# Kernel optimization log

Hardware: AMD Instinct MI355X
Metric: run time of the kernel (lower is better)

The kernel has to match this reference:

```python
import jax, jax.numpy as jnp
import numpy as np

EPS_T = 0.008856  # CIE threshold


def _f(t):
    # torch.where(t > 0.008856, t**(1/3), 7.787*t + 16/116)
    safe = jnp.where(t > EPS_T, t, 1.0)  # avoid nan/inf grads in untaken branch
    return jnp.where(t > EPS_T, jnp.cbrt(safe), 7.787 * t + 16.0 / 116.0)


def rgb_to_cieluv(rgb):
    # rgb: (N, 3, H, W) -> (N, 3, H, W) with channels (L, u, v)
    r, g, b = rgb[:, 0], rgb[:, 1], rgb[:, 2]
    x = 0.4124564 * r + 0.3575761 * g + 0.1804375 * b
    y = 0.2126729 * r + 0.7151522 * g + 0.072175 * b
    z = 0.0193339 * r + 0.119192 * g + 0.9503041 * b
    x = x / 0.95047
    z = z / 1.08883
    fx, fy, fz = _f(x), _f(y), _f(z)
    l = 116.0 * fy - 16.0
    u = 13.0 * l * (fx - fy)
    v = 13.0 * l * (fy - fz)
    return jnp.stack([l, u, v], axis=1)


def box_filter(img, patch_size):
    # depthwise all-ones conv, same padding as torch (pad = k//2)
    c = img.shape[1]
    kernel = jnp.ones((c, 1, patch_size, patch_size), img.dtype)
    pad = patch_size // 2
    return jax.lax.conv_general_dilated(
        img, kernel, window_strides=(1, 1),
        padding=[(pad, pad), (pad, pad)], feature_group_count=c)


def setup_inputs() -> dict:
    key = jax.random.key(0)
    k1, k2 = jax.random.split(key)
    N, C, H, W = 16, 3, 512, 512
    inp = jax.random.uniform(k1, (N, C, H, W), dtype=jnp.float32)
    tgt = jax.random.uniform(k2, (N, C, H, W), dtype=jnp.float32)
    return {"input": inp, "target": tgt, "patch_size": 15}


def reference(input, target, patch_size):
    a = box_filter(rgb_to_cieluv(input), patch_size)
    b = box_filter(rgb_to_cieluv(target), patch_size)
    # l_loss + u_loss + v_loss: per-channel MSE, summed across channels
    per_channel_mse = jnp.mean((a - b) ** 2, axis=(0, 2, 3))
    return per_channel_mse.sum()
```

## Files before the change

kernel.cpp:

```cpp
#include <hip/hip_runtime.h>
#include <math.h>

#define IMG_W 512
#define IMG_H 512
#define NIMG 16
#define HWSZ (IMG_W * IMG_H)
#define CHWSZ (3 * HWSZ)
#define NORM (1.0 / 4194304.0)
#define NBLK_V 1536

__device__ __forceinline__ float f_lab(float t) {
    float c = exp2f(log2f(t) * (1.0f / 3.0f));
    return (t > 0.008856f) ? c : fmaf(7.787f, t, 0.13793103448275862f);
}

__device__ __forceinline__ void rgb_to_luv(float r, float g, float b,
                                           float& l, float& u, float& v) {
    float x = 0.4124564f * r + 0.3575761f * g + 0.1804375f * b;
    float y = 0.2126729f * r + 0.7151522f * g + 0.0721750f * b;
    float z = 0.0193339f * r + 0.1191920f * g + 0.9503041f * b;
    x *= (1.0f / 0.95047f);
    z *= (1.0f / 1.08883f);
    float fx = f_lab(x), fy = f_lab(y), fz = f_lab(z);
    l = 116.0f * fy - 16.0f;
    u = 13.0f * l * (fx - fy);
    v = 13.0f * l * (fy - fz);
}

__device__ __forceinline__ unsigned short f2bf(float x) {
    unsigned int u = __float_as_uint(x);
    u += 0x7fff + ((u >> 16) & 1);
    return (unsigned short)(u >> 16);
}

__device__ __forceinline__ void hslide(const float d[8], float o[8], int lane) {
    float L[7], R[7];
    #pragma unroll
    for (int j = 0; j < 7; ++j) {
        float l = __shfl_up(d[j + 1], 1, 64);
        L[j] = (lane == 0) ? 0.0f : l;
        float r = __shfl_down(d[j], 1, 64);
        R[j] = (lane == 63) ? 0.0f : r;
    }
    float s = 0.0f;
    #pragma unroll
    for (int j = 0; j < 7; ++j) s += L[j];
    #pragma unroll
    for (int j = 0; j < 8; ++j) s += d[j];
    o[0] = s;
    #pragma unroll
    for (int k = 1; k < 8; ++k) o[k] = o[k - 1] + R[k - 1] - L[k - 1];
}

__device__ __forceinline__ uint4 pack8(const float o[8]) {
    uint4 p;
    p.x = (unsigned)f2bf(o[0]) | ((unsigned)f2bf(o[1]) << 16);
    p.y = (unsigned)f2bf(o[2]) | ((unsigned)f2bf(o[3]) << 16);
    p.z = (unsigned)f2bf(o[4]) | ((unsigned)f2bf(o[5]) << 16);
    p.w = (unsigned)f2bf(o[6]) | ((unsigned)f2bf(o[7]) << 16);
    return p;
}

__global__ __launch_bounds__(256) void luv_hpass3(
        const float* __restrict__ inp, const float* __restrict__ tgt,
        unsigned short* __restrict__ tmp) {
    int blk = blockIdx.x;
    int n = blk >> 7;
    int lane = threadIdx.x & 63;
    int h = ((blk & 127) << 2) | (threadIdx.x >> 6);
    int w0 = lane << 3;
    size_t base = (size_t)n * CHWSZ + (size_t)h * IMG_W + w0;

    float dl[8], du[8], dv[8];
    {
        float R[8], G[8], B[8];
        *(float4*)&R[0] = *(const float4*)(inp + base);
        *(float4*)&R[4] = *(const float4*)(inp + base + 4);
        *(float4*)&G[0] = *(const float4*)(inp + base + HWSZ);
        *(float4*)&G[4] = *(const float4*)(inp + base + HWSZ + 4);
        *(float4*)&B[0] = *(const float4*)(inp + base + 2 * HWSZ);
        *(float4*)&B[4] = *(const float4*)(inp + base + 2 * HWSZ + 4);
        #pragma unroll
        for (int j = 0; j < 8; ++j)
            rgb_to_luv(R[j], G[j], B[j], dl[j], du[j], dv[j]);
        *(float4*)&R[0] = *(const float4*)(tgt + base);
        *(float4*)&R[4] = *(const float4*)(tgt + base + 4);
        *(float4*)&G[0] = *(const float4*)(tgt + base + HWSZ);
        *(float4*)&G[4] = *(const float4*)(tgt + base + HWSZ + 4);
        *(float4*)&B[0] = *(const float4*)(tgt + base + 2 * HWSZ);
        *(float4*)&B[4] = *(const float4*)(tgt + base + 2 * HWSZ + 4);
        #pragma unroll
        for (int j = 0; j < 8; ++j) {
            float l2, u2, v2;
            rgb_to_luv(R[j], G[j], B[j], l2, u2, v2);
            dl[j] -= l2; du[j] -= u2; dv[j] -= v2;
        }
    }

    float o[8];
    hslide(dl, o, lane);
    *reinterpret_cast<uint4*>(tmp + base) = pack8(o);
    hslide(du, o, lane);
    *reinterpret_cast<uint4*>(tmp + base + HWSZ) = pack8(o);
    hslide(dv, o, lane);
    *reinterpret_cast<uint4*>(tmp + base + 2 * HWSZ) = pack8(o);
}

__device__ __forceinline__ void unpack8(uint4 v, float f[8]) {
    f[0] = __uint_as_float(v.x << 16);
    f[1] = __uint_as_float(v.x & 0xffff0000u);
    f[2] = __uint_as_float(v.y << 16);
    f[3] = __uint_as_float(v.y & 0xffff0000u);
    f[4] = __uint_as_float(v.z << 16);
    f[5] = __uint_as_float(v.z & 0xffff0000u);
    f[6] = __uint_as_float(v.w << 16);
    f[7] = __uint_as_float(v.w & 0xffff0000u);
}

template <bool GLO>
__device__ __forceinline__ void vprime(const unsigned short* __restrict__ col,
                                       int h0, float W[8]) {
    #pragma unroll
    for (int j = 0; j < 15; ++j) {
        int h = h0 - 7 + j;
        if (GLO && h < 0) continue;
        uint4 v = *(const uint4*)(col + (size_t)h * IMG_W);
        float a[8];
        unpack8(v, a);
        #pragma unroll
        for (int c = 0; c < 8; ++c) W[c] += a[c];
    }
}

template <bool GLO, bool GHI>
__device__ __forceinline__ void vchunk8(const unsigned short* __restrict__ col,
                                        int hb, float W[8], float& acc) {
    const uint4 z = make_uint4(0u, 0u, 0u, 0u);
    uint4 va[8], vs[8];
    #pragma unroll
    for (int j = 0; j < 8; ++j) {
        int ha = hb + j + 8, hs = hb + j - 7;
        va[j] = (GHI && ha >= IMG_H) ? z : *(const uint4*)(col + (size_t)ha * IMG_W);
        vs[j] = (GLO && hs < 0)      ? z : *(const uint4*)(col + (size_t)hs * IMG_W);
    }
    #pragma unroll
    for (int j = 0; j < 8; ++j) {
        float a[8], s[8];
        unpack8(va[j], a);
        unpack8(vs[j], s);
        #pragma unroll
        for (int c = 0; c < 8; ++c) {
            acc += W[c] * W[c];
            W[c] += a[c] - s[c];
        }
    }
}

__global__ __launch_bounds__(64) void vpass3(
        const unsigned short* __restrict__ tmp, float* __restrict__ partial) {
    int blk = blockIdx.x;
    int hseg = blk & 31;
    int nc = blk >> 5;
    int t = threadIdx.x;
    const unsigned short* col = tmp + (size_t)nc * HWSZ + (t << 3);
    int h0 = hseg << 4;

    float W[8] = {0.f, 0.f, 0.f, 0.f, 0.f, 0.f, 0.f, 0.f};
    float acc = 0.0f;

    if (hseg == 0) {
        vprime<true>(col, h0, W);
        vchunk8<true, false>(col, h0, W, acc);
        vchunk8<false, false>(col, h0 + 8, W, acc);
    } else if (hseg == 31) {
        vprime<false>(col, h0, W);
        vchunk8<false, false>(col, h0, W, acc);
        vchunk8<false, true>(col, h0 + 8, W, acc);
    } else {
        vprime<false>(col, h0, W);
        vchunk8<false, false>(col, h0, W, acc);
        vchunk8<false, false>(col, h0 + 8, W, acc);
    }

    #pragma unroll
    for (int off = 32; off > 0; off >>= 1)
        acc += __shfl_down(acc, off, 64);
    if (t == 0) partial[blk] = acc;
}

__global__ __launch_bounds__(256) void finalize3(
        const float* __restrict__ partial, float* __restrict__ out) {
    int t = threadIdx.x;
    float a = 0.0f;
    #pragma unroll
    for (int i = 0; i < NBLK_V; i += 256) a += partial[i + t];
    #pragma unroll
    for (int off = 32; off > 0; off >>= 1)
        a += __shfl_down(a, off, 64);
    __shared__ float red[4];
    int lane = t & 63, wid = t >> 6;
    if (lane == 0) red[wid] = a;
    __syncthreads();
    if (t == 0)
        out[0] = (float)((double)(red[0] + red[1] + red[2] + red[3]) * NORM);
}

extern "C" void kernel_launch(void* const* d_in, const int* in_sizes, int n_in,
                              void* d_out, int out_size, void* d_ws, size_t ws_size,
                              hipStream_t stream) {
    const float* inp = (const float*)d_in[0];
    const float* tgt = (const float*)d_in[1];
    float* out = (float*)d_out;
    float* partial = (float*)d_ws;
    unsigned short* tmp = (unsigned short*)((char*)d_ws + 8192);

    luv_hpass3<<<NIMG * 128, 256, 0, stream>>>(inp, tgt, tmp);
    vpass3<<<NBLK_V, 64, 0, stream>>>(tmp, partial);
    finalize3<<<1, 256, 0, stream>>>(partial, out);
}
```

Before: 133.6 us.

## Fuse LUV conversion and box filter into one kernel with shared-memory ring

Merges the horizontal-pass and vertical-pass kernels into one kernel. Each block converts rows to LUV differences, horizontally box-filters them into a bf16 ring buffer in LDS, and slides the vertical window there. This removes the global bf16 intermediate write and its repeated reads, plus one launch. In exchange it recomputes halo rows per 32-row tile, launches only 256 large blocks, and adds block-wide barriers inside the loop.

```diff
diff --git a/kernel.cpp b/kernel.cpp
--- a/kernel.cpp
+++ b/kernel.cpp
@@ -7,7 +7,8 @@
 #define HWSZ (IMG_W * IMG_H)
 #define CHWSZ (3 * HWSZ)
 #define NORM (1.0 / 4194304.0)
-#define NBLK_V 1536
+#define RING 24
+#define NBLK 256
 
 __device__ __forceinline__ float f_lab(float t) {
     float c = exp2f(log2f(t) * (1.0f / 3.0f));
@@ -32,6 +33,9 @@
     u += 0x7fff + ((u >> 16) & 1);
     return (unsigned short)(u >> 16);
 }
+__device__ __forceinline__ float bf2f(unsigned short u) {
+    return __uint_as_float((unsigned)u << 16);
+}
 
 __device__ __forceinline__ void hslide(const float d[8], float o[8], int lane) {
     float L[7], R[7];
@@ -61,139 +65,126 @@
     return p;
 }
 
-__global__ __launch_bounds__(256) void luv_hpass3(
-        const float* __restrict__ inp, const float* __restrict__ tgt,
-        unsigned short* __restrict__ tmp) {
-    int blk = blockIdx.x;
-    int n = blk >> 7;
-    int lane = threadIdx.x & 63;
-    int h = ((blk & 127) << 2) | (threadIdx.x >> 6);
+__device__ __forceinline__ void load6(const float* __restrict__ p, size_t base,
+                                      float4 v[6]) {
+    v[0] = *(const float4*)(p + base);
+    v[1] = *(const float4*)(p + base + 4);
+    v[2] = *(const float4*)(p + base + HWSZ);
+    v[3] = *(const float4*)(p + base + HWSZ + 4);
+    v[4] = *(const float4*)(p + base + 2 * HWSZ);
+    v[5] = *(const float4*)(p + base + 2 * HWSZ + 4);
+}
+
+__device__ __forceinline__ void row_to_ring(const float4 vi[6], const float4 vt[6],
+        bool valid, unsigned short (*ring)[3][IMG_W], int slot, int lane) {
     int w0 = lane << 3;
-    size_t base = (size_t)n * CHWSZ + (size_t)h * IMG_W + w0;
-
-    float dl[8], du[8], dv[8];
-    {
-        float R[8], G[8], B[8];
-        *(float4*)&R[0] = *(const float4*)(inp + base);
-        *(float4*)&R[4] = *(const float4*)(inp + base + 4);
-        *(float4*)&G[0] = *(const float4*)(inp + base + HWSZ);
-        *(float4*)&G[4] = *(const float4*)(inp + base + HWSZ + 4);
-        *(float4*)&B[0] = *(const float4*)(inp + base + 2 * HWSZ);
-        *(float4*)&B[4] = *(const float4*)(inp + base + 2 * HWSZ + 4);
+    if (valid) {
+        float R[8], G[8], B[8], dl[8], du[8], dv[8];
+        *(float4*)&R[0] = vi[0]; *(float4*)&R[4] = vi[1];
+        *(float4*)&G[0] = vi[2]; *(float4*)&G[4] = vi[3];
+        *(float4*)&B[0] = vi[4]; *(float4*)&B[4] = vi[5];
         #pragma unroll
         for (int j = 0; j < 8; ++j)
             rgb_to_luv(R[j], G[j], B[j], dl[j], du[j], dv[j]);
-        *(float4*)&R[0] = *(const float4*)(tgt + base);
-        *(float4*)&R[4] = *(const float4*)(tgt + base + 4);
-        *(float4*)&G[0] = *(const float4*)(tgt + base + HWSZ);
-        *(float4*)&G[4] = *(const float4*)(tgt + base + HWSZ + 4);
-        *(float4*)&B[0] = *(const float4*)(tgt + base + 2 * HWSZ);
-        *(float4*)&B[4] = *(const float4*)(tgt + base + 2 * HWSZ + 4);
+        *(float4*)&R[0] = vt[0]; *(float4*)&R[4] = vt[1];
+        *(float4*)&G[0] = vt[2]; *(float4*)&G[4] = vt[3];
+        *(float4*)&B[0] = vt[4]; *(float4*)&B[4] = vt[5];
         #pragma unroll
         for (int j = 0; j < 8; ++j) {
             float l2, u2, v2;
             rgb_to_luv(R[j], G[j], B[j], l2, u2, v2);
             dl[j] -= l2; du[j] -= u2; dv[j] -= v2;
         }
-    }
-
-    float o[8];
-    hslide(dl, o, lane);
-    *reinterpret_cast<uint4*>(tmp + base) = pack8(o);
-    hslide(du, o, lane);
-    *reinterpret_cast<uint4*>(tmp + base + HWSZ) = pack8(o);
-    hslide(dv, o, lane);
-    *reinterpret_cast<uint4*>(tmp + base + 2 * HWSZ) = pack8(o);
-}
-
-__device__ __forceinline__ void unpack8(uint4 v, float f[8]) {
-    f[0] = __uint_as_float(v.x << 16);
-    f[1] = __uint_as_float(v.x & 0xffff0000u);
-    f[2] = __uint_as_float(v.y << 16);
-    f[3] = __uint_as_float(v.y & 0xffff0000u);
-    f[4] = __uint_as_float(v.z << 16);
-    f[5] = __uint_as_float(v.z & 0xffff0000u);
-    f[6] = __uint_as_float(v.w << 16);
-    f[7] = __uint_as_float(v.w & 0xffff0000u);
-}
-
-template <bool GLO>
-__device__ __forceinline__ void vprime(const unsigned short* __restrict__ col,
-                                       int h0, float W[8]) {
-    #pragma unroll
-    for (int j = 0; j < 15; ++j) {
-        int h = h0 - 7 + j;
-        if (GLO && h < 0) continue;
-        uint4 v = *(const uint4*)(col + (size_t)h * IMG_W);
-        float a[8];
-        unpack8(v, a);
-        #pragma unroll
-        for (int c = 0; c < 8; ++c) W[c] += a[c];
-    }
-}
-
-template <bool GLO, bool GHI>
-__device__ __forceinline__ void vchunk8(const unsigned short* __restrict__ col,
-                                        int hb, float W[8], float& acc) {
-    const uint4 z = make_uint4(0u, 0u, 0u, 0u);
-    uint4 va[8], vs[8];
-    #pragma unroll
-    for (int j = 0; j < 8; ++j) {
-        int ha = hb + j + 8, hs = hb + j - 7;
-        va[j] = (GHI && ha >= IMG_H) ? z : *(const uint4*)(col + (size_t)ha * IMG_W);
-        vs[j] = (GLO && hs < 0)      ? z : *(const uint4*)(col + (size_t)hs * IMG_W);
-    }
-    #pragma unroll
-    for (int j = 0; j < 8; ++j) {
-        float a[8], s[8];
-        unpack8(va[j], a);
-        unpack8(vs[j], s);
-        #pragma unroll
-        for (int c = 0; c < 8; ++c) {
-            acc += W[c] * W[c];
-            W[c] += a[c] - s[c];
+        float o[8];
+        hslide(dl, o, lane); *(uint4*)&ring[slot][0][w0] = pack8(o);
+        hslide(du, o, lane); *(uint4*)&ring[slot][1][w0] = pack8(o);
+        hslide(dv, o, lane); *(uint4*)&ring[slot][2][w0] = pack8(o);
+    } else {
+        uint4 z = make_uint4(0u, 0u, 0u, 0u);
+        *(uint4*)&ring[slot][0][w0] = z;
+        *(uint4*)&ring[slot][1][w0] = z;
+        *(uint4*)&ring[slot][2][w0] = z;
+    }
+}
+
+__global__ __launch_bounds__(512) void fused_luv_box(
+        const float* __restrict__ inp, const float* __restrict__ tgt,
+        float* __restrict__ partial) {
+    __shared__ unsigned short ring[RING][3][IMG_W];
+    __shared__ float red[8];
+    int blk = blockIdx.x;
+    int n = blk >> 4;
+    int h0 = (blk & 15) << 5;
+    int t = (int)threadIdx.x;
+    int wid = t >> 6, lane = t & 63;
+    int w0 = lane << 3;
+    size_t nb = (size_t)n * CHWSZ + w0;
+
+    float4 xa[6], xb[6], ya[6], yb[6];
+    int pr0 = h0 - 7 + wid;
+    int pr1 = pr0 + 8, pr2 = pr0 + 16;
+    bool v0 = (pr0 >= 0);
+    if (v0) { load6(inp, nb + (size_t)pr0 * IMG_W, xa);
+              load6(tgt, nb + (size_t)pr0 * IMG_W, xb); }
+    load6(inp, nb + (size_t)pr1 * IMG_W, ya);
+    load6(tgt, nb + (size_t)pr1 * IMG_W, yb);
+    row_to_ring(xa, xb, v0, ring, wid, lane);
+    load6(inp, nb + (size_t)pr2 * IMG_W, xa);
+    load6(tgt, nb + (size_t)pr2 * IMG_W, xb);
+    row_to_ring(ya, yb, true, ring, 8 + wid, lane);
+    row_to_ring(xa, xb, true, ring, 16 + wid, lane);
+    __syncthreads();
+
+    int col = t;
+    float Wl = 0.f, Wu = 0.f, Wv = 0.f;
+    #pragma unroll
+    for (int r = 0; r < 15; ++r) {
+        Wl += bf2f(ring[r][0][col]);
+        Wu += bf2f(ring[r][1][col]);
+        Wv += bf2f(ring[r][2][col]);
+    }
+
+    float acc = 0.f;
+    #pragma unroll
+    for (int b = 0; b < 4; ++b) {
+        bool hasG = (b < 3);
+        int pr = h0 + 17 + 8 * b + wid;
+        bool gv = hasG && (pr < IMG_H) && (b < 2 || wid < 6);
+        if (gv) { load6(inp, nb + (size_t)pr * IMG_W, xa);
+                  load6(tgt, nb + (size_t)pr * IMG_W, xb); }
+        #pragma unroll
+        for (int j = 0; j < 8; ++j) {
+            int i = 8 * b + j;
+            acc += Wl * Wl + Wu * Wu + Wv * Wv;
+            if (i < 31) {
+                int sA = (i + 15) % 24, sS = i % 24;
+                Wl += bf2f(ring[sA][0][col]) - bf2f(ring[sS][0][col]);
+                Wu += bf2f(ring[sA][1][col]) - bf2f(ring[sS][1][col]);
+                Wv += bf2f(ring[sA][2][col]) - bf2f(ring[sS][2][col]);
+            }
         }
-    }
-}
-
-__global__ __launch_bounds__(64) void vpass3(
-        const unsigned short* __restrict__ tmp, float* __restrict__ partial) {
-    int blk = blockIdx.x;
-    int hseg = blk & 31;
-    int nc = blk >> 5;
-    int t = threadIdx.x;
-    const unsigned short* col = tmp + (size_t)nc * HWSZ + (t << 3);
-    int h0 = hseg << 4;
-
-    float W[8] = {0.f, 0.f, 0.f, 0.f, 0.f, 0.f, 0.f, 0.f};
-    float acc = 0.0f;
-
-    if (hseg == 0) {
-        vprime<true>(col, h0, W);
-        vchunk8<true, false>(col, h0, W, acc);
-        vchunk8<false, false>(col, h0 + 8, W, acc);
-    } else if (hseg == 31) {
-        vprime<false>(col, h0, W);
-        vchunk8<false, false>(col, h0, W, acc);
-        vchunk8<false, true>(col, h0 + 8, W, acc);
-    } else {
-        vprime<false>(col, h0, W);
-        vchunk8<false, false>(col, h0, W, acc);
-        vchunk8<false, false>(col, h0 + 8, W, acc);
+        __syncthreads();
+        if (hasG) row_to_ring(xa, xb, gv, ring, 8 * b + wid, lane);
+        __syncthreads();
     }
 
     #pragma unroll
     for (int off = 32; off > 0; off >>= 1)
         acc += __shfl_down(acc, off, 64);
-    if (t == 0) partial[blk] = acc;
-}
-
-__global__ __launch_bounds__(256) void finalize3(
+    if (lane == 0) red[wid] = acc;
+    __syncthreads();
+    if (t == 0) {
+        float s = 0.f;
+        #pragma unroll
+        for (int k = 0; k < 8; ++k) s += red[k];
+        partial[blk] = s;
+    }
+}
+
+__global__ __launch_bounds__(256) void finalize4(
         const float* __restrict__ partial, float* __restrict__ out) {
-    int t = threadIdx.x;
-    float a = 0.0f;
-    #pragma unroll
-    for (int i = 0; i < NBLK_V; i += 256) a += partial[i + t];
+    int t = (int)threadIdx.x;
+    float a = partial[t];
     #pragma unroll
     for (int off = 32; off > 0; off >>= 1)
         a += __shfl_down(a, off, 64);
@@ -212,9 +203,7 @@
     const float* tgt = (const float*)d_in[1];
     float* out = (float*)d_out;
     float* partial = (float*)d_ws;
-    unsigned short* tmp = (unsigned short*)((char*)d_ws + 8192);
-
-    luv_hpass3<<<NIMG * 128, 256, 0, stream>>>(inp, tgt, tmp);
-    vpass3<<<NBLK_V, 64, 0, stream>>>(tmp, partial);
-    finalize3<<<1, 256, 0, stream>>>(partial, out);
-}
+
+    fused_luv_box<<<NBLK, 512, 0, stream>>>(inp, tgt, partial);
+    finalize4<<<1, 256, 0, stream>>>(partial, out);
+}
```

Measured after the change: 150.2 us. 1.12x slower.

## Fuse final reduction into vertical pass via atomic ticket and narrow column tiles

Applied to the files above, without the earlier changes.

Drops the separate finalize kernel by having each vertical-pass block atomically add its partial sum and bump a counter, with the last block writing the normalized result. The accumulator and counter are reset inside the first kernel. The vertical pass is also re-tiled so each thread handles 4 columns over 32 rows instead of 8 columns over 16 rows, which halves how often the 14-row priming overlap is re-read. The float atomic accumulation makes the summation order nondeterministic and adds contention on one address. It also relies on the first kernel fully finishing before the second starts.

```diff
diff --git a/kernel.cpp b/kernel.cpp
--- a/kernel.cpp
+++ b/kernel.cpp
@@ -63,8 +63,10 @@
 
 __global__ __launch_bounds__(256) void luv_hpass3(
         const float* __restrict__ inp, const float* __restrict__ tgt,
-        unsigned short* __restrict__ tmp) {
+        unsigned short* __restrict__ tmp, float* __restrict__ acc,
+        unsigned int* __restrict__ cnt) {
     int blk = blockIdx.x;
+    if (blk == 0 && threadIdx.x == 0) { acc[0] = 0.0f; cnt[0] = 0u; }
     int n = blk >> 7;
     int lane = threadIdx.x & 63;
     int h = ((blk & 127) << 2) | (threadIdx.x >> 6);
@@ -106,103 +108,100 @@
     *reinterpret_cast<uint4*>(tmp + base + 2 * HWSZ) = pack8(o);
 }
 
-__device__ __forceinline__ void unpack8(uint4 v, float f[8]) {
+__device__ __forceinline__ void unpack4(uint2 v, float f[4]) {
     f[0] = __uint_as_float(v.x << 16);
     f[1] = __uint_as_float(v.x & 0xffff0000u);
     f[2] = __uint_as_float(v.y << 16);
     f[3] = __uint_as_float(v.y & 0xffff0000u);
-    f[4] = __uint_as_float(v.z << 16);
-    f[5] = __uint_as_float(v.z & 0xffff0000u);
-    f[6] = __uint_as_float(v.w << 16);
-    f[7] = __uint_as_float(v.w & 0xffff0000u);
 }
 
 template <bool GLO>
-__device__ __forceinline__ void vprime(const unsigned short* __restrict__ col,
-                                       int h0, float W[8]) {
+__device__ __forceinline__ void vprime4(const unsigned short* __restrict__ col,
+                                        int h0, float W[4]) {
     #pragma unroll
     for (int j = 0; j < 15; ++j) {
         int h = h0 - 7 + j;
         if (GLO && h < 0) continue;
-        uint4 v = *(const uint4*)(col + (size_t)h * IMG_W);
-        float a[8];
-        unpack8(v, a);
-        #pragma unroll
-        for (int c = 0; c < 8; ++c) W[c] += a[c];
+        uint2 v = *(const uint2*)(col + (size_t)h * IMG_W);
+        float a[4];
+        unpack4(v, a);
+        #pragma unroll
+        for (int c = 0; c < 4; ++c) W[c] += a[c];
     }
 }
 
 template <bool GLO, bool GHI>
-__device__ __forceinline__ void vchunk8(const unsigned short* __restrict__ col,
-                                        int hb, float W[8], float& acc) {
-    const uint4 z = make_uint4(0u, 0u, 0u, 0u);
-    uint4 va[8], vs[8];
+__device__ __forceinline__ void vchunk8_4(const unsigned short* __restrict__ col,
+                                          int hb, float W[4], float& acc) {
+    const uint2 z = make_uint2(0u, 0u);
+    uint2 va[8], vs[8];
     #pragma unroll
     for (int j = 0; j < 8; ++j) {
         int ha = hb + j + 8, hs = hb + j - 7;
-        va[j] = (GHI && ha >= IMG_H) ? z : *(const uint4*)(col + (size_t)ha * IMG_W);
-        vs[j] = (GLO && hs < 0)      ? z : *(const uint4*)(col + (size_t)hs * IMG_W);
+        va[j] = (GHI && ha >= IMG_H) ? z : *(const uint2*)(col + (size_t)ha * IMG_W);
+        vs[j] = (GLO && hs < 0)      ? z : *(const uint2*)(col + (size_t)hs * IMG_W);
     }
     #pragma unroll
     for (int j = 0; j < 8; ++j) {
-        float a[8], s[8];
-        unpack8(va[j], a);
-        unpack8(vs[j], s);
-        #pragma unroll
-        for (int c = 0; c < 8; ++c) {
+        float a[4], s[4];
+        unpack4(va[j], a);
+        unpack4(vs[j], s);
+        #pragma unroll
+        for (int c = 0; c < 4; ++c) {
             acc += W[c] * W[c];
             W[c] += a[c] - s[c];
         }
     }
 }
 
-__global__ __launch_bounds__(64) void vpass3(
-        const unsigned short* __restrict__ tmp, float* __restrict__ partial) {
+__global__ __launch_bounds__(64) void vpass4(
+        const unsigned short* __restrict__ tmp, float* __restrict__ acc,
+        unsigned int* __restrict__ cnt, float* __restrict__ out) {
     int blk = blockIdx.x;
-    int hseg = blk & 31;
+    int half = blk & 1;
+    int seg = (blk >> 1) & 15;
     int nc = blk >> 5;
-    int t = threadIdx.x;
-    const unsigned short* col = tmp + (size_t)nc * HWSZ + (t << 3);
-    int h0 = hseg << 4;
-
-    float W[8] = {0.f, 0.f, 0.f, 0.f, 0.f, 0.f, 0.f, 0.f};
-    float acc = 0.0f;
-
-    if (hseg == 0) {
-        vprime<true>(col, h0, W);
-        vchunk8<true, false>(col, h0, W, acc);
-        vchunk8<false, false>(col, h0 + 8, W, acc);
-    } else if (hseg == 31) {
-        vprime<false>(col, h0, W);
-        vchunk8<false, false>(col, h0, W, acc);
-        vchunk8<false, true>(col, h0 + 8, W, acc);
+    int t = (int)threadIdx.x;
+    const unsigned short* col = tmp + (size_t)nc * HWSZ + (half << 8) + (t << 2);
+    int h0 = seg << 5;
+
+    float W[4] = {0.f, 0.f, 0.f, 0.f};
+    float a = 0.0f;
+
+    if (seg == 0) {
+        vprime4<true>(col, h0, W);
+        vchunk8_4<true,  false>(col, h0,      W, a);
+        vchunk8_4<false, false>(col, h0 + 8,  W, a);
+        vchunk8_4<false, false>(col, h0 + 16, W, a);
+        vchunk8_4<false, false>(col, h0 + 24, W, a);
+    } else if (seg == 15) {
+        vprime4<false>(col, h0, W);
+        vchunk8_4<false, false>(col, h0,      W, a);
+        vchunk8_4<false, false>(col, h0 + 8,  W, a);
+        vchunk8_4<false, false>(col, h0 + 16, W, a);
+        vchunk8_4<false, true >(col, h0 + 24, W, a);
     } else {
-        vprime<false>(col, h0, W);
-        vchunk8<false, false>(col, h0, W, acc);
-        vchunk8<false, false>(col, h0 + 8, W, acc);
-    }
-
-    #pragma unroll
-    for (int off = 32; off > 0; off >>= 1)
-        acc += __shfl_down(acc, off, 64);
-    if (t == 0) partial[blk] = acc;
-}
-
-__global__ __launch_bounds__(256) void finalize3(
-        const float* __restrict__ partial, float* __restrict__ out) {
-    int t = threadIdx.x;
-    float a = 0.0f;
-    #pragma unroll
-    for (int i = 0; i < NBLK_V; i += 256) a += partial[i + t];
+        vprime4<false>(col, h0, W);
+        vchunk8_4<false, false>(col, h0,      W, a);
+        vchunk8_4<false, false>(col, h0 + 8,  W, a);
+        vchunk8_4<false, false>(col, h0 + 16, W, a);
+        vchunk8_4<false, false>(col, h0 + 24, W, a);
+    }
+
     #pragma unroll
     for (int off = 32; off > 0; off >>= 1)
         a += __shfl_down(a, off, 64);
-    __shared__ float red[4];
-    int lane = t & 63, wid = t >> 6;
-    if (lane == 0) red[wid] = a;
-    __syncthreads();
-    if (t == 0)
-        out[0] = (float)((double)(red[0] + red[1] + red[2] + red[3]) * NORM);
+
+    if (t == 0) {
+        atomicAdd(acc, a);
+        __threadfence();
+        unsigned int ticket = atomicAdd(cnt, 1u);
+        if (ticket == NBLK_V - 1) {
+            __threadfence();
+            float s = atomicAdd(acc, 0.0f);
+            out[0] = (float)((double)s * NORM);
+        }
+    }
 }
 
 extern "C" void kernel_launch(void* const* d_in, const int* in_sizes, int n_in,
@@ -211,10 +210,10 @@
     const float* inp = (const float*)d_in[0];
     const float* tgt = (const float*)d_in[1];
     float* out = (float*)d_out;
-    float* partial = (float*)d_ws;
-    unsigned short* tmp = (unsigned short*)((char*)d_ws + 8192);
-
-    luv_hpass3<<<NIMG * 128, 256, 0, stream>>>(inp, tgt, tmp);
-    vpass3<<<NBLK_V, 64, 0, stream>>>(tmp, partial);
-    finalize3<<<1, 256, 0, stream>>>(partial, out);
-}
+    float* acc = (float*)d_ws;
+    unsigned int* cnt = (unsigned int*)((char*)d_ws + 64);
+    unsigned short* tmp = (unsigned short*)((char*)d_ws + 4096);
+
+    luv_hpass3<<<NIMG * 128, 256, 0, stream>>>(inp, tgt, tmp, acc, cnt);
+    vpass4<<<NBLK_V, 64, 0, stream>>>(tmp, acc, cnt, out);
+}
```

New measurement: 162.3 us. +21.5%, slower.

## Fuse final reduction into vertical pass with atomics and shorter row segments

Applied to the files above, without the earlier changes.

Drops the separate finalize kernel: each vertical-pass block atomically adds its partial sum, and the last block, found through a ticket counter, writes the result. The vertical pass now runs 256-thread blocks with four waves, each covering an 8-row segment instead of 16, which gives more parallelism at the cost of more redundant 15-row priming loads. The horizontal pass issues all input and target loads up front to overlap memory latency. Float atomic accumulation makes the summation order nondeterministic.

```diff
diff --git a/kernel.cpp b/kernel.cpp
--- a/kernel.cpp
+++ b/kernel.cpp
@@ -7,7 +7,7 @@
 #define HWSZ (IMG_W * IMG_H)
 #define CHWSZ (3 * HWSZ)
 #define NORM (1.0 / 4194304.0)
-#define NBLK_V 1536
+#define NBLK_V 768
 
 __device__ __forceinline__ float f_lab(float t) {
     float c = exp2f(log2f(t) * (1.0f / 3.0f));
@@ -61,40 +61,39 @@
     return p;
 }
 
-__global__ __launch_bounds__(256) void luv_hpass3(
+__global__ __launch_bounds__(256) void luv_hpass5(
         const float* __restrict__ inp, const float* __restrict__ tgt,
-        unsigned short* __restrict__ tmp) {
+        unsigned short* __restrict__ tmp, float* __restrict__ acc,
+        unsigned int* __restrict__ cnt) {
     int blk = blockIdx.x;
+    if (blk == 0 && threadIdx.x == 0) { acc[0] = 0.0f; cnt[0] = 0u; }
     int n = blk >> 7;
     int lane = threadIdx.x & 63;
     int h = ((blk & 127) << 2) | (threadIdx.x >> 6);
     int w0 = lane << 3;
     size_t base = (size_t)n * CHWSZ + (size_t)h * IMG_W + w0;
 
+    float R1[8], G1[8], B1[8], R2[8], G2[8], B2[8];
+    *(float4*)&R1[0] = *(const float4*)(inp + base);
+    *(float4*)&R1[4] = *(const float4*)(inp + base + 4);
+    *(float4*)&G1[0] = *(const float4*)(inp + base + HWSZ);
+    *(float4*)&G1[4] = *(const float4*)(inp + base + HWSZ + 4);
+    *(float4*)&B1[0] = *(const float4*)(inp + base + 2 * HWSZ);
+    *(float4*)&B1[4] = *(const float4*)(inp + base + 2 * HWSZ + 4);
+    *(float4*)&R2[0] = *(const float4*)(tgt + base);
+    *(float4*)&R2[4] = *(const float4*)(tgt + base + 4);
+    *(float4*)&G2[0] = *(const float4*)(tgt + base + HWSZ);
+    *(float4*)&G2[4] = *(const float4*)(tgt + base + HWSZ + 4);
+    *(float4*)&B2[0] = *(const float4*)(tgt + base + 2 * HWSZ);
+    *(float4*)&B2[4] = *(const float4*)(tgt + base + 2 * HWSZ + 4);
+
     float dl[8], du[8], dv[8];
-    {
-        float R[8], G[8], B[8];
-        *(float4*)&R[0] = *(const float4*)(inp + base);
-        *(float4*)&R[4] = *(const float4*)(inp + base + 4);
-        *(float4*)&G[0] = *(const float4*)(inp + base + HWSZ);
-        *(float4*)&G[4] = *(const float4*)(inp + base + HWSZ + 4);
-        *(float4*)&B[0] = *(const float4*)(inp + base + 2 * HWSZ);
-        *(float4*)&B[4] = *(const float4*)(inp + base + 2 * HWSZ + 4);
-        #pragma unroll
-        for (int j = 0; j < 8; ++j)
-            rgb_to_luv(R[j], G[j], B[j], dl[j], du[j], dv[j]);
-        *(float4*)&R[0] = *(const float4*)(tgt + base);
-        *(float4*)&R[4] = *(const float4*)(tgt + base + 4);
-        *(float4*)&G[0] = *(const float4*)(tgt + base + HWSZ);
-        *(float4*)&G[4] = *(const float4*)(tgt + base + HWSZ + 4);
-        *(float4*)&B[0] = *(const float4*)(tgt + base + 2 * HWSZ);
-        *(float4*)&B[4] = *(const float4*)(tgt + base + 2 * HWSZ + 4);
-        #pragma unroll
-        for (int j = 0; j < 8; ++j) {
-            float l2, u2, v2;
-            rgb_to_luv(R[j], G[j], B[j], l2, u2, v2);
-            dl[j] -= l2; du[j] -= u2; dv[j] -= v2;
-        }
+    #pragma unroll
+    for (int j = 0; j < 8; ++j) {
+        float l1, u1, v1, l2, u2, v2;
+        rgb_to_luv(R1[j], G1[j], B1[j], l1, u1, v1);
+        rgb_to_luv(R2[j], G2[j], B2[j], l2, u2, v2);
+        dl[j] = l1 - l2; du[j] = u1 - u2; dv[j] = v1 - v2;
     }
 
     float o[8];
@@ -117,92 +116,78 @@
     f[7] = __uint_as_float(v.w & 0xffff0000u);
 }
 
-template <bool GLO>
-__device__ __forceinline__ void vprime(const unsigned short* __restrict__ col,
-                                       int h0, float W[8]) {
+template <bool GLO, bool GHI>
+__device__ __forceinline__ float vseg8(const unsigned short* __restrict__ col,
+                                       int h0) {
+    const uint4 z = make_uint4(0u, 0u, 0u, 0u);
+    float W[8] = {0.f, 0.f, 0.f, 0.f, 0.f, 0.f, 0.f, 0.f};
     #pragma unroll
     for (int j = 0; j < 15; ++j) {
-        int h = h0 - 7 + j;
-        if (GLO && h < 0) continue;
-        uint4 v = *(const uint4*)(col + (size_t)h * IMG_W);
+        int hh = h0 - 7 + j;
+        if (GLO && hh < 0) continue;
+        uint4 v = *(const uint4*)(col + (size_t)hh * IMG_W);
         float a[8];
         unpack8(v, a);
         #pragma unroll
         for (int c = 0; c < 8; ++c) W[c] += a[c];
     }
-}
-
-template <bool GLO, bool GHI>
-__device__ __forceinline__ void vchunk8(const unsigned short* __restrict__ col,
-                                        int hb, float W[8], float& acc) {
-    const uint4 z = make_uint4(0u, 0u, 0u, 0u);
-    uint4 va[8], vs[8];
-    #pragma unroll
-    for (int j = 0; j < 8; ++j) {
-        int ha = hb + j + 8, hs = hb + j - 7;
+    uint4 va[7], vs[7];
+    #pragma unroll
+    for (int j = 0; j < 7; ++j) {
+        int ha = h0 + 8 + j, hs = h0 - 7 + j;
         va[j] = (GHI && ha >= IMG_H) ? z : *(const uint4*)(col + (size_t)ha * IMG_W);
         vs[j] = (GLO && hs < 0)      ? z : *(const uint4*)(col + (size_t)hs * IMG_W);
     }
+    float acc = 0.f;
     #pragma unroll
     for (int j = 0; j < 8; ++j) {
-        float a[8], s[8];
-        unpack8(va[j], a);
-        unpack8(vs[j], s);
         #pragma unroll
-        for (int c = 0; c < 8; ++c) {
-            acc += W[c] * W[c];
-            W[c] += a[c] - s[c];
+        for (int c = 0; c < 8; ++c) acc += W[c] * W[c];
+        if (j < 7) {
+            float a[8], s[8];
+            unpack8(va[j], a);
+            unpack8(vs[j], s);
+            #pragma unroll
+            for (int c = 0; c < 8; ++c) W[c] += a[c] - s[c];
         }
     }
-}
-
-__global__ __launch_bounds__(64) void vpass3(
-        const unsigned short* __restrict__ tmp, float* __restrict__ partial) {
-    int blk = blockIdx.x;
-    int hseg = blk & 31;
-    int nc = blk >> 5;
-    int t = threadIdx.x;
-    const unsigned short* col = tmp + (size_t)nc * HWSZ + (t << 3);
-    int h0 = hseg << 4;
-
-    float W[8] = {0.f, 0.f, 0.f, 0.f, 0.f, 0.f, 0.f, 0.f};
-    float acc = 0.0f;
-
-    if (hseg == 0) {
-        vprime<true>(col, h0, W);
-        vchunk8<true, false>(col, h0, W, acc);
-        vchunk8<false, false>(col, h0 + 8, W, acc);
-    } else if (hseg == 31) {
-        vprime<false>(col, h0, W);
-        vchunk8<false, false>(col, h0, W, acc);
-        vchunk8<false, true>(col, h0 + 8, W, acc);
-    } else {
-        vprime<false>(col, h0, W);
-        vchunk8<false, false>(col, h0, W, acc);
-        vchunk8<false, false>(col, h0 + 8, W, acc);
-    }
-
-    #pragma unroll
-    for (int off = 32; off > 0; off >>= 1)
-        acc += __shfl_down(acc, off, 64);
-    if (t == 0) partial[blk] = acc;
-}
-
-__global__ __launch_bounds__(256) void finalize3(
-        const float* __restrict__ partial, float* __restrict__ out) {
-    int t = threadIdx.x;
-    float a = 0.0f;
-    #pragma unroll
-    for (int i = 0; i < NBLK_V; i += 256) a += partial[i + t];
+    return acc;
+}
+
+__global__ __launch_bounds__(256) void vpass5(
+        const unsigned short* __restrict__ tmp, float* __restrict__ acc,
+        unsigned int* __restrict__ cnt, float* __restrict__ out) {
+    int t = (int)threadIdx.x;
+    int wid = t >> 6, lane = t & 63;
+    int g = (blockIdx.x << 2) | wid;
+    int nc = g >> 6;
+    int seg = g & 63;
+    const unsigned short* col = tmp + (size_t)nc * HWSZ + (lane << 3);
+    int h0 = seg << 3;
+
+    float a;
+    if (seg == 0)       a = vseg8<true,  false>(col, h0);
+    else if (seg == 63) a = vseg8<false, true >(col, h0);
+    else                a = vseg8<false, false>(col, h0);
+
     #pragma unroll
     for (int off = 32; off > 0; off >>= 1)
         a += __shfl_down(a, off, 64);
+
     __shared__ float red[4];
-    int lane = t & 63, wid = t >> 6;
     if (lane == 0) red[wid] = a;
     __syncthreads();
-    if (t == 0)
-        out[0] = (float)((double)(red[0] + red[1] + red[2] + red[3]) * NORM);
+    if (t == 0) {
+        float s = red[0] + red[1] + red[2] + red[3];
+        atomicAdd(acc, s);
+        __threadfence();
+        unsigned int ticket = atomicAdd(cnt, 1u);
+        if (ticket == NBLK_V - 1) {
+            __threadfence();
+            float tot = atomicAdd(acc, 0.0f);
+            out[0] = (float)((double)tot * NORM);
+        }
+    }
 }
 
 extern "C" void kernel_launch(void* const* d_in, const int* in_sizes, int n_in,
@@ -211,10 +196,10 @@
     const float* inp = (const float*)d_in[0];
     const float* tgt = (const float*)d_in[1];
     float* out = (float*)d_out;
-    float* partial = (float*)d_ws;
-    unsigned short* tmp = (unsigned short*)((char*)d_ws + 8192);
-
-    luv_hpass3<<<NIMG * 128, 256, 0, stream>>>(inp, tgt, tmp);
-    vpass3<<<NBLK_V, 64, 0, stream>>>(tmp, partial);
-    finalize3<<<1, 256, 0, stream>>>(partial, out);
-}
+    float* acc = (float*)d_ws;
+    unsigned int* cnt = (unsigned int*)((char*)d_ws + 64);
+    unsigned short* tmp = (unsigned short*)((char*)d_ws + 4096);
+
+    luv_hpass5<<<NIMG * 128, 256, 0, stream>>>(inp, tgt, tmp, acc, cnt);
+    vpass5<<<NBLK_V, 256, 0, stream>>>(tmp, acc, cnt, out);
+}
```

Result: slower. 148.5 us (+11.2%).
